# Performance work log

Hardware: AMD Instinct MI355X
Metric: run time of the kernel (lower is better)

## Reference

```python
import jax, jax.numpy as jnp
import numpy as np

B, N0, D0, N1, D1 = 128, 64, 32, 64, 32
K = 65  # depthwise conv kernel size
SCALE = 5.0
FOCUS = 3.0
EPS_Z = float(jnp.finfo(jnp.float32).eps)


def setup_inputs() -> dict:
    key = jax.random.key(0)
    k1, k2, k3, kw, kc, kb = jax.random.split(key, 6)
    x1 = jax.random.normal(k1, (B, N0, D0), dtype=jnp.float32)
    x2 = jax.random.normal(k2, (B, N0, D0), dtype=jnp.float32)
    x3 = jax.random.normal(k3, (B, N0, D0), dtype=jnp.float32)
    # kaiming_normal_ on W [N1, N0, D0, D1]: fan_in = N0*D0*D1 per torch default on 4D
    fan_in = N0 * D0 * D1
    W = jax.random.normal(kw, (N1, N0, D0, D1), dtype=jnp.float32) * np.sqrt(2.0 / fan_in)
    # Conv1d(N1*D1, N1*D1, K, groups=N1): weight [out_ch, in_ch/groups, K]
    cin_g = D1
    bound = 1.0 / np.sqrt(cin_g * K)
    conv_w = jax.random.uniform(kc, (N1 * D1, cin_g, K), dtype=jnp.float32, minval=-bound, maxval=bound)
    conv_b = jax.random.uniform(kb, (N1 * D1,), dtype=jnp.float32, minval=-bound, maxval=bound)
    return {"x1": x1, "x2": x2, "x3": x3, "W": W, "conv_w": conv_w, "conv_b": conv_b}


def _transform(x, W):
    # x: [B, N0, D0], W: [N1, N0, D0, D1] -> u: [B, N1*D1, N0]
    u = jnp.einsum('bji,kjiz->bkjz', x, W)        # [B, N1, N0, D1]
    u = jnp.transpose(u, (0, 1, 3, 2))             # [B, N1, D1, N0]
    return u.reshape(u.shape[0], N1 * D1, N0)


def _focus(u):
    # ReLU kernel + focusing-factor renormalization along last dim
    u = jax.nn.relu(u) + 1e-6
    u = u / SCALE
    n = jnp.linalg.norm(u, axis=-1, keepdims=True)
    up = u ** FOCUS
    return up / jnp.linalg.norm(up, axis=-1, keepdims=True) * n


def _squash(x, eps=1e-20):
    norm = jnp.linalg.norm(x, axis=-1, keepdims=True)
    coef = 1.0 - 1.0 / (jnp.exp(norm) + eps)
    return coef * (x / (norm + eps))


def reference(x1, x2, x3, W, conv_w, conv_b):
    u1 = _focus(_transform(x1, W))  # [B, N1*D1, N0]
    u2 = _focus(_transform(x2, W))
    u3 = _focus(_transform(x3, W))
    z = 1.0 / (jnp.einsum('bic,bc->bi', u1, u1.sum(axis=1)) + EPS_Z)  # [B, N1*D1]
    kv = jnp.einsum('bjc,bjd->bcd', u2, u3)                           # [B, N0, N0]
    x = jnp.einsum('bic,bcd,bi->bid', u1, kv, z)                      # [B, N1*D1, N0]
    # grouped (depthwise-per-capsule) conv1d, 'same' padding
    y = jax.lax.conv_general_dilated(
        x, conv_w, window_strides=(1,), padding=[(K // 2, K // 2)],
        dimension_numbers=('NCH', 'OIH', 'NCH'), feature_group_count=N1)
    y = y + conv_b[None, :, None]
    out = (x + y).sum(axis=-1).reshape(-1, N1, D1)  # [B, N1, D1]
    return _squash(out)
```

## Files before the change

### kernel.cpp

```cpp
#include <hip/hip_runtime.h>
#include <cstddef>

#define NB 128
#define NT 64
#define ND 32
#define NG 64
#define NC 2048
#define KW 65
#define EPSZ 1.1920928955078125e-07f

#define OFF_URAW 0ull
#define SZ_URAW  (3ull * NB * NT * NC)
#define OFF_F    (OFF_URAW + SZ_URAW)
#define SZ_F     (3ull * NB * NC)
#define OFF_S1   (OFF_F + SZ_F)
#define SZ_S1    ((unsigned long long)NB * NT)
#define OFF_KV   (OFF_S1 + SZ_S1)
#define SZ_KV    ((unsigned long long)NB * NT * NT)

__device__ __forceinline__ float foc(float v, float fv) {
  float u = (fmaxf(v, 0.f) + 1e-6f) * 0.2f;
  return u * u * u * fv;
}

__global__ __launch_bounds__(256) void k_transform(
    const float* __restrict__ x1, const float* __restrict__ x2,
    const float* __restrict__ x3, const float* __restrict__ W,
    float* __restrict__ uraw) {
  int bid = blockIdx.x;
  int j   = bid & 63;
  int nt  = (bid >> 6) & 15;
  int inp = bid >> 10;
  const float* x = (inp == 0) ? x1 : ((inp == 1) ? x2 : x3);
  float* uout = uraw + (size_t)inp * ((size_t)NB * NT * NC);

  __shared__ float as[32][132];
  __shared__ float bs[32][132];
  int tid = threadIdx.x;

  {
    int b = tid >> 1, h = tid & 1;
    const float* xp = x + ((size_t)b * NT + j) * ND + h * 16;
#pragma unroll
    for (int q = 0; q < 4; ++q) {
      float4 v = *reinterpret_cast<const float4*>(xp + q * 4);
      int i0 = h * 16 + q * 4;
      as[i0 + 0][b] = v.x; as[i0 + 1][b] = v.y;
      as[i0 + 2][b] = v.z; as[i0 + 3][b] = v.w;
    }
  }
  {
    int kk = tid >> 6, u = tid & 63;
    int i = u >> 1, h = u & 1;
    const float* wp = W + (((size_t)(nt * 4 + kk) * NT + j) * ND + i) * ND + h * 16;
#pragma unroll
    for (int q = 0; q < 4; ++q) {
      float4 v = *reinterpret_cast<const float4*>(wp + q * 4);
      int c0 = kk * 32 + h * 16 + q * 4;
      bs[i][c0 + 0] = v.x; bs[i][c0 + 1] = v.y;
      bs[i][c0 + 2] = v.z; bs[i][c0 + 3] = v.w;
    }
  }
  __syncthreads();

  int tm = tid & 15, tn = tid >> 4;
  int m0 = tm * 8, n0 = tn * 8;
  float acc[8][8];
#pragma unroll
  for (int a = 0; a < 8; ++a)
#pragma unroll
    for (int c = 0; c < 8; ++c) acc[a][c] = 0.f;

#pragma unroll 4
  for (int kk = 0; kk < 32; ++kk) {
    float4 a0 = *reinterpret_cast<const float4*>(&as[kk][m0]);
    float4 a1 = *reinterpret_cast<const float4*>(&as[kk][m0 + 4]);
    float4 b0 = *reinterpret_cast<const float4*>(&bs[kk][n0]);
    float4 b1 = *reinterpret_cast<const float4*>(&bs[kk][n0 + 4]);
    float av[8] = {a0.x, a0.y, a0.z, a0.w, a1.x, a1.y, a1.z, a1.w};
    float bv[8] = {b0.x, b0.y, b0.z, b0.w, b1.x, b1.y, b1.z, b1.w};
#pragma unroll
    for (int mi = 0; mi < 8; ++mi)
#pragma unroll
      for (int ni = 0; ni < 8; ++ni)
        acc[mi][ni] = fmaf(av[mi], bv[ni], acc[mi][ni]);
  }

#pragma unroll
  for (int mi = 0; mi < 8; ++mi) {
    float* cp = uout + ((size_t)(m0 + mi) * NT + j) * NC + nt * 128 + n0;
    float4 v0 = {acc[mi][0], acc[mi][1], acc[mi][2], acc[mi][3]};
    float4 v1 = {acc[mi][4], acc[mi][5], acc[mi][6], acc[mi][7]};
    *reinterpret_cast<float4*>(cp)     = v0;
    *reinterpret_cast<float4*>(cp + 4) = v1;
  }
}

__global__ __launch_bounds__(256) void k_factors(
    const float* __restrict__ uraw, float* __restrict__ f,
    float* __restrict__ s1) {
  int bid = blockIdx.x;
  int q = bid & 3, b = (bid >> 2) & 127, inp = bid >> 9;
  const float* u = uraw + ((size_t)inp * NB + b) * ((size_t)NT * NC);
  int tid = threadIdx.x;
  int ch = q * 512 + tid * 2;

  float s2a = 0.f, s6a = 0.f, s2b = 0.f, s6b = 0.f;
  for (int t = 0; t < NT; ++t) {
    float2 v = *reinterpret_cast<const float2*>(u + (size_t)t * NC + ch);
    float ua = (fmaxf(v.x, 0.f) + 1e-6f) * 0.2f;
    float p2a = ua * ua, p3a = p2a * ua;
    s2a += p2a; s6a += p3a * p3a;
    float ub = (fmaxf(v.y, 0.f) + 1e-6f) * 0.2f;
    float p2b = ub * ub, p3b = p2b * ub;
    s2b += p2b; s6b += p3b * p3b;
  }
  float fa = sqrtf(s2a) / sqrtf(s6a);
  float fb = sqrtf(s2b) / sqrtf(s6b);
  float2 fv = {fa, fb};
  *reinterpret_cast<float2*>(f + ((size_t)inp * NB + b) * NC + ch) = fv;

  if (inp == 0) {
    __shared__ float part[NT][4];
    int wid = tid >> 6, lane = tid & 63;
    for (int t = 0; t < NT; ++t) {
      float2 v = *reinterpret_cast<const float2*>(u + (size_t)t * NC + ch);
      float ua = (fmaxf(v.x, 0.f) + 1e-6f) * 0.2f;
      float ub = (fmaxf(v.y, 0.f) + 1e-6f) * 0.2f;
      float val = ua * ua * ua * fa + ub * ub * ub * fb;
#pragma unroll
      for (int m = 32; m >= 1; m >>= 1) val += __shfl_xor(val, m, 64);
      if (lane == 0) part[t][wid] = val;
    }
    __syncthreads();
    if (tid < NT)
      atomicAdd(&s1[b * NT + tid],
                part[tid][0] + part[tid][1] + part[tid][2] + part[tid][3]);
  }
}

__global__ void k_zero(float* __restrict__ p, int n) {
  int i = blockIdx.x * blockDim.x + threadIdx.x;
  int stride = gridDim.x * blockDim.x;
  for (; i < n; i += stride) p[i] = 0.f;
}

__global__ __launch_bounds__(256) void k_kv(
    const float* __restrict__ uraw, const float* __restrict__ f,
    float* __restrict__ kv) {
  int b = blockIdx.x >> 2, ks = blockIdx.x & 3;
  int wv = threadIdx.x >> 6, lane = threadIdx.x & 63;
  const float* u2 = uraw + ((size_t)NB + b) * ((size_t)NT * NC);
  const float* u3 = uraw + (2ull * NB + b) * ((size_t)NT * NC);
  const float* f2 = f + ((size_t)NB + b) * NC;
  const float* f3 = f + (2ull * NB + b) * NC;

  __shared__ float ldsF[16384];
  float* L2 = ldsF + wv * 4096;
  float* L3 = L2 + 2048;

  int tm = lane >> 3, tn = lane & 7;
  int sr = lane >> 3, c4 = lane & 7;

  float acc[8][8];
#pragma unroll
  for (int i = 0; i < 8; ++i)
#pragma unroll
    for (int j = 0; j < 8; ++j) acc[i][j] = 0.f;

  for (int chunk = 0; chunk < 4; ++chunk) {
    int ch0 = ks * 512 + wv * 128 + chunk * 32;
    float4 f2q = *reinterpret_cast<const float4*>(f2 + ch0 + c4 * 4);
    float4 f3q = *reinterpret_cast<const float4*>(f3 + ch0 + c4 * 4);
#pragma unroll
    for (int it = 0; it < 8; ++it) {
      int t = it * 8 + sr;
      int q4s = c4 ^ sr ^ it;
      float4 v2 = *reinterpret_cast<const float4*>(u2 + (size_t)t * NC + ch0 + c4 * 4);
      float4 v3 = *reinterpret_cast<const float4*>(u3 + (size_t)t * NC + ch0 + c4 * 4);
      float4 w2 = {foc(v2.x, f2q.x), foc(v2.y, f2q.y), foc(v2.z, f2q.z), foc(v2.w, f2q.w)};
      float4 w3 = {foc(v3.x, f3q.x), foc(v3.y, f3q.y), foc(v3.z, f3q.z), foc(v3.w, f3q.w)};
      *reinterpret_cast<float4*>(L2 + t * 32 + q4s * 4) = w2;
      *reinterpret_cast<float4*>(L3 + t * 32 + q4s * 4) = w3;
    }

#pragma unroll
    for (int kp = 0; kp < 16; ++kp) {
      int q4 = kp >> 1, h = (kp & 1) * 2;
      float2 af[8], bf[8];
#pragma unroll
      for (int i = 0; i < 8; ++i)
        af[i] = *reinterpret_cast<const float2*>(
            L2 + (tm * 8 + i) * 32 + ((q4 ^ i ^ tm) * 4 + h));
#pragma unroll
      for (int j = 0; j < 8; ++j)
        bf[j] = *reinterpret_cast<const float2*>(
            L3 + (tn * 8 + j) * 32 + ((q4 ^ j ^ tn) * 4 + h));
#pragma unroll
      for (int i = 0; i < 8; ++i)
#pragma unroll
        for (int j = 0; j < 8; ++j)
          acc[i][j] = fmaf(af[i].y, bf[j].y, fmaf(af[i].x, bf[j].x, acc[i][j]));
    }
  }

  __syncthreads();
  if (wv > 0) {
    float* dp = ldsF + (wv - 1) * 4224 + lane * 66;
#pragma unroll
    for (int i = 0; i < 8; ++i)
#pragma unroll
      for (int j = 0; j < 8; ++j) dp[i * 8 + j] = acc[i][j];
  }
  __syncthreads();
  if (wv == 0) {
    float* kvp = kv + (size_t)b * (NT * NT);
    const float* d0 = ldsF + lane * 66;
    const float* d1 = ldsF + 4224 + lane * 66;
    const float* d2 = ldsF + 8448 + lane * 66;
#pragma unroll
    for (int i = 0; i < 8; ++i)
#pragma unroll
      for (int j = 0; j < 8; ++j) {
        int c = i * 8 + j;
        atomicAdd(&kvp[(tm * 8 + i) * 64 + tn * 8 + j],
                  acc[i][j] + d0[c] + d1[c] + d2[c]);
      }
  }
}

__global__ __launch_bounds__(64) void k_cwt(
    const float* __restrict__ cw, float* __restrict__ cwt) {
  int o = blockIdx.x;
  int tid = threadIdx.x;
  __shared__ float row[32 * KW];
  for (int i = tid; i < 32 * KW; i += 64) row[i] = cw[(size_t)o * (32 * KW) + i];
  __syncthreads();
  int jj = tid, j = jj + 1;
  for (int ci = 0; ci < 32; ++ci) {
    float v = 0.f;
    if (j <= 32) v -= row[ci * KW + j + 32];
    if (j >= 32 && j <= 63) v += row[ci * KW + j - 32];
    if (j == 64) {
      float s = 0.f;
      for (int k = 32; k <= 64; ++k) s += row[ci * KW + k];
      v += s;
    }
    cwt[(size_t)o * 2048 + ci * 64 + jj] = v;
  }
}

__global__ __launch_bounds__(256) void k_pre(
    const float* __restrict__ uraw, const float* __restrict__ f,
    const float* __restrict__ kvg, const float* __restrict__ s1g,
    float* __restrict__ pre) {
  int b = blockIdx.x >> 3, q = blockIdx.x & 7;
  int chbase = q * 256;
  const float* u1 = uraw + (size_t)b * ((size_t)NT * NC);
  const float* f1 = f + (size_t)b * NC;
  int tid = threadIdx.x;

  __shared__ float kvpreL[64][68];
  __shared__ float s1L[64];
  __shared__ float utL[64][132];

#pragma unroll
  for (int qq = 0; qq < 16; ++qq) {
    int i = tid + qq * 256;
    kvpreL[i >> 6][i & 63] = kvg[(size_t)b * (NT * NT) + i];
  }
  if (tid < 64) s1L[tid] = s1g[b * NT + tid];
  __syncthreads();
  if (tid < 64) {
    float run = 0.f;
    for (int t2 = 0; t2 < 64; ++t2) {
      run += kvpreL[tid][t2];
      kvpreL[tid][t2] = run;
    }
  }

  int cg = tid >> 3, tg = tid & 7;
  for (int tile = 0; tile < 2; ++tile) {
    int ch0 = chbase + tile * 128;
    __syncthreads();
    {
      int t = tid >> 2, c4 = tid & 3;
      const float* up = u1 + (size_t)t * NC + ch0 + c4 * 32;
      const float* fp = f1 + ch0 + c4 * 32;
#pragma unroll
      for (int qq = 0; qq < 8; ++qq) {
        float4 v  = *reinterpret_cast<const float4*>(up + qq * 4);
        float4 fv = *reinterpret_cast<const float4*>(fp + qq * 4);
        float vv[4] = {v.x, v.y, v.z, v.w};
        float ff[4] = {fv.x, fv.y, fv.z, fv.w};
#pragma unroll
        for (int r = 0; r < 4; ++r) {
          float uu = (fmaxf(vv[r], 0.f) + 1e-6f) * 0.2f;
          utL[t][c4 * 33 + qq * 4 + r] = uu * uu * uu * ff[r];
        }
      }
    }
    __syncthreads();

    int cl = cg * 4;
    int sk = (cl >> 5) * 33 + (cl & 31);
    float acc[4][8];
#pragma unroll
    for (int r = 0; r < 4; ++r)
#pragma unroll
      for (int c = 0; c < 8; ++c) acc[r][c] = 0.f;
    float accz[4] = {0.f, 0.f, 0.f, 0.f};

#pragma unroll 4
    for (int t1 = 0; t1 < 64; ++t1) {
      float4 a = *reinterpret_cast<const float4*>(&utL[t1][sk]);
      float s = s1L[t1];
      float4 k0 = *reinterpret_cast<const float4*>(&kvpreL[t1][tg * 8]);
      float4 k1 = *reinterpret_cast<const float4*>(&kvpreL[t1][tg * 8 + 4]);
      float aa[4] = {a.x, a.y, a.z, a.w};
      float kk[8] = {k0.x, k0.y, k0.z, k0.w, k1.x, k1.y, k1.z, k1.w};
#pragma unroll
      for (int r = 0; r < 4; ++r) {
        accz[r] = fmaf(aa[r], s, accz[r]);
#pragma unroll
        for (int c = 0; c < 8; ++c)
          acc[r][c] = fmaf(aa[r], kk[c], acc[r][c]);
      }
    }
#pragma unroll
    for (int r = 0; r < 4; ++r) {
      float z = 1.f / (accz[r] + EPSZ);
      float* pp = pre + ((size_t)b * NC + ch0 + cl + r) * 64 + tg * 8;
      float4 o0 = {acc[r][0] * z, acc[r][1] * z, acc[r][2] * z, acc[r][3] * z};
      float4 o1 = {acc[r][4] * z, acc[r][5] * z, acc[r][6] * z, acc[r][7] * z};
      *reinterpret_cast<float4*>(pp)     = o0;
      *reinterpret_cast<float4*>(pp + 4) = o1;
    }
  }
}

__global__ __launch_bounds__(256) void k_gemm(
    const float* __restrict__ pre, const float* __restrict__ cwt,
    const float* __restrict__ cb, float* __restrict__ out) {
  int g = blockIdx.x >> 2, bq = blockIdx.x & 3;
  int b0 = bq * 32;
  int tid = threadIdx.x;
  int oh = tid & 15, bh = tid >> 4;

  __shared__ float preL[32][68];
  __shared__ float cwtL[32][68];

  float a00 = 0.f, a01 = 0.f, a10 = 0.f, a11 = 0.f;
  float xs00 = 0.f, xs01 = 0.f, xs10 = 0.f, xs11 = 0.f;

  for (int kc = 0; kc < 32; ++kc) {
    __syncthreads();
    {
      int r8 = tid >> 3, s8 = tid & 7;
      const float* ps = pre + ((size_t)(b0 + r8) * NC + g * 32) * 64 + kc * 64 + s8 * 8;
      float4 p0 = *reinterpret_cast<const float4*>(ps);
      float4 p1 = *reinterpret_cast<const float4*>(ps + 4);
      *reinterpret_cast<float4*>(&preL[r8][s8 * 8])     = p0;
      *reinterpret_cast<float4*>(&preL[r8][s8 * 8 + 4]) = p1;
      const float* cs = cwt + (size_t)(g * 32 + r8) * 2048 + kc * 64 + s8 * 8;
      float4 c0 = *reinterpret_cast<const float4*>(cs);
      float4 c1 = *reinterpret_cast<const float4*>(cs + 4);
      *reinterpret_cast<float4*>(&cwtL[r8][s8 * 8])     = c0;
      *reinterpret_cast<float4*>(&cwtL[r8][s8 * 8 + 4]) = c1;
    }
    __syncthreads();

    if (kc == oh)      { xs00 = preL[bh][63]; xs10 = preL[bh + 16][63]; }
    if (kc == oh + 16) { xs01 = preL[bh][63]; xs11 = preL[bh + 16][63]; }

#pragma unroll
    for (int kk = 0; kk < 64; kk += 4) {
      float4 p0 = *reinterpret_cast<const float4*>(&preL[bh][kk]);
      float4 p1 = *reinterpret_cast<const float4*>(&preL[bh + 16][kk]);
      float4 c0 = *reinterpret_cast<const float4*>(&cwtL[oh][kk]);
      float4 c1 = *reinterpret_cast<const float4*>(&cwtL[oh + 16][kk]);
      a00 = fmaf(p0.x, c0.x, a00); a00 = fmaf(p0.y, c0.y, a00);
      a00 = fmaf(p0.z, c0.z, a00); a00 = fmaf(p0.w, c0.w, a00);
      a01 = fmaf(p0.x, c1.x, a01); a01 = fmaf(p0.y, c1.y, a01);
      a01 = fmaf(p0.z, c1.z, a01); a01 = fmaf(p0.w, c1.w, a01);
      a10 = fmaf(p1.x, c0.x, a10); a10 = fmaf(p1.y, c0.y, a10);
      a10 = fmaf(p1.z, c0.z, a10); a10 = fmaf(p1.w, c0.w, a10);
      a11 = fmaf(p1.x, c1.x, a11); a11 = fmaf(p1.y, c1.y, a11);
      a11 = fmaf(p1.z, c1.z, a11); a11 = fmaf(p1.w, c1.w, a11);
    }
  }

  float cb0 = cb[g * 32 + oh], cb1 = cb[g * 32 + oh + 16];
  float v00 = a00 + xs00 + 64.f * cb0;
  float v01 = a01 + xs01 + 64.f * cb1;
  float v10 = a10 + xs10 + 64.f * cb0;
  float v11 = a11 + xs11 + 64.f * cb1;

  float sqA = v00 * v00 + v01 * v01;
  float sqB = v10 * v10 + v11 * v11;
#pragma unroll
  for (int m = 8; m >= 1; m >>= 1) {
    sqA += __shfl_xor(sqA, m, 16);
    sqB += __shfl_xor(sqB, m, 16);
  }
  float nA = sqrtf(sqA), nB = sqrtf(sqB);
  float cA = 1.f - 1.f / (expf(nA) + 1e-20f);
  float cB = 1.f - 1.f / (expf(nB) + 1e-20f);
  float iA = cA / (nA + 1e-20f), iB = cB / (nB + 1e-20f);

  size_t baseA = ((size_t)(b0 + bh) * NG + g) * ND;
  size_t baseB = ((size_t)(b0 + bh + 16) * NG + g) * ND;
  out[baseA + oh]      = v00 * iA;
  out[baseA + oh + 16] = v01 * iA;
  out[baseB + oh]      = v10 * iB;
  out[baseB + oh + 16] = v11 * iB;
}

extern "C" void kernel_launch(void* const* d_in, const int* in_sizes, int n_in,
                              void* d_out, int out_size, void* d_ws, size_t ws_size,
                              hipStream_t stream) {
  const float* x1 = (const float*)d_in[0];
  const float* x2 = (const float*)d_in[1];
  const float* x3 = (const float*)d_in[2];
  const float* W  = (const float*)d_in[3];
  const float* cw = (const float*)d_in[4];
  const float* cb = (const float*)d_in[5];
  float* out = (float*)d_out;

  float* ws   = (float*)d_ws;
  float* uraw = ws + OFF_URAW;
  float* f    = ws + OFF_F;
  float* s1   = ws + OFF_S1;
  float* kv   = ws + OFF_KV;
  float* pre  = uraw + (size_t)NB * NT * NC;
  float* cwt  = uraw + 2ull * NB * NT * NC;

  k_transform<<<3072, 256, 0, stream>>>(x1, x2, x3, W, uraw);
  k_zero<<<256, 256, 0, stream>>>(s1, (int)(SZ_S1 + SZ_KV));
  k_factors<<<1536, 256, 0, stream>>>(uraw, f, s1);
  k_kv<<<512, 256, 0, stream>>>(uraw, f, kv);
  k_cwt<<<2048, 64, 0, stream>>>(cw, cwt);
  k_pre<<<1024, 256, 0, stream>>>(uraw, f, kv, s1, pre);
  k_gemm<<<256, 256, 0, stream>>>(pre, cwt, cb, out);
}
```

Baseline: 422.9 us.

## Fuse focus-factor computation for inputs 2 and 3 into the kv kernel

After: 412.0 us. 1.03x faster.

```diff
diff --git a/kernel.cpp b/kernel.cpp
--- a/kernel.cpp
+++ b/kernel.cpp
@@ -100,8 +100,8 @@
     const float* __restrict__ uraw, float* __restrict__ f,
     float* __restrict__ s1) {
   int bid = blockIdx.x;
-  int q = bid & 3, b = (bid >> 2) & 127, inp = bid >> 9;
-  const float* u = uraw + ((size_t)inp * NB + b) * ((size_t)NT * NC);
+  int q = bid & 3, b = bid >> 2;
+  const float* u = uraw + (size_t)b * ((size_t)NT * NC);
   int tid = threadIdx.x;
   int ch = q * 512 + tid * 2;
 
@@ -118,25 +118,23 @@
   float fa = sqrtf(s2a) / sqrtf(s6a);
   float fb = sqrtf(s2b) / sqrtf(s6b);
   float2 fv = {fa, fb};
-  *reinterpret_cast<float2*>(f + ((size_t)inp * NB + b) * NC + ch) = fv;
-
-  if (inp == 0) {
-    __shared__ float part[NT][4];
-    int wid = tid >> 6, lane = tid & 63;
-    for (int t = 0; t < NT; ++t) {
-      float2 v = *reinterpret_cast<const float2*>(u + (size_t)t * NC + ch);
-      float ua = (fmaxf(v.x, 0.f) + 1e-6f) * 0.2f;
-      float ub = (fmaxf(v.y, 0.f) + 1e-6f) * 0.2f;
-      float val = ua * ua * ua * fa + ub * ub * ub * fb;
-#pragma unroll
-      for (int m = 32; m >= 1; m >>= 1) val += __shfl_xor(val, m, 64);
-      if (lane == 0) part[t][wid] = val;
-    }
-    __syncthreads();
-    if (tid < NT)
-      atomicAdd(&s1[b * NT + tid],
-                part[tid][0] + part[tid][1] + part[tid][2] + part[tid][3]);
-  }
+  *reinterpret_cast<float2*>(f + (size_t)b * NC + ch) = fv;
+
+  __shared__ float part[NT][4];
+  int wid = tid >> 6, lane = tid & 63;
+  for (int t = 0; t < NT; ++t) {
+    float2 v = *reinterpret_cast<const float2*>(u + (size_t)t * NC + ch);
+    float ua = (fmaxf(v.x, 0.f) + 1e-6f) * 0.2f;
+    float ub = (fmaxf(v.y, 0.f) + 1e-6f) * 0.2f;
+    float val = ua * ua * ua * fa + ub * ub * ub * fb;
+#pragma unroll
+    for (int m = 32; m >= 1; m >>= 1) val += __shfl_xor(val, m, 64);
+    if (lane == 0) part[t][wid] = val;
+  }
+  __syncthreads();
+  if (tid < NT)
+    atomicAdd(&s1[b * NT + tid],
+              part[tid][0] + part[tid][1] + part[tid][2] + part[tid][3]);
 }
 
 __global__ void k_zero(float* __restrict__ p, int n) {
@@ -146,87 +144,105 @@
 }
 
 __global__ __launch_bounds__(256) void k_kv(
-    const float* __restrict__ uraw, const float* __restrict__ f,
-    float* __restrict__ kv) {
-  int b = blockIdx.x >> 2, ks = blockIdx.x & 3;
-  int wv = threadIdx.x >> 6, lane = threadIdx.x & 63;
+    const float* __restrict__ uraw, float* __restrict__ kv) {
+  int b = blockIdx.x >> 3, ks = blockIdx.x & 7;
+  int tid = threadIdx.x;
+  int wv = tid >> 6, lane = tid & 63;
   const float* u2 = uraw + ((size_t)NB + b) * ((size_t)NT * NC);
   const float* u3 = uraw + (2ull * NB + b) * ((size_t)NT * NC);
-  const float* f2 = f + ((size_t)NB + b) * NC;
-  const float* f3 = f + (2ull * NB + b) * NC;
-
-  __shared__ float ldsF[16384];
-  float* L2 = ldsF + wv * 4096;
-  float* L3 = L2 + 2048;
-
+
+  __shared__ float L[2][64][32];
+  __shared__ float fL[2][32];
+
+  int q4 = tid & 7, tr = tid >> 3;
+  int colf = tid >> 1, hf = tid & 1;
+  int opf = colf >> 5, chf = colf & 31, c4f = chf >> 2, clf = chf & 3;
+  int qr = wv >> 1, qc = wv & 1;
   int tm = lane >> 3, tn = lane & 7;
-  int sr = lane >> 3, c4 = lane & 7;
-
-  float acc[8][8];
-#pragma unroll
-  for (int i = 0; i < 8; ++i)
-#pragma unroll
-    for (int j = 0; j < 8; ++j) acc[i][j] = 0.f;
-
-  for (int chunk = 0; chunk < 4; ++chunk) {
-    int ch0 = ks * 512 + wv * 128 + chunk * 32;
-    float4 f2q = *reinterpret_cast<const float4*>(f2 + ch0 + c4 * 4);
-    float4 f3q = *reinterpret_cast<const float4*>(f3 + ch0 + c4 * 4);
-#pragma unroll
-    for (int it = 0; it < 8; ++it) {
-      int t = it * 8 + sr;
-      int q4s = c4 ^ sr ^ it;
-      float4 v2 = *reinterpret_cast<const float4*>(u2 + (size_t)t * NC + ch0 + c4 * 4);
-      float4 v3 = *reinterpret_cast<const float4*>(u3 + (size_t)t * NC + ch0 + c4 * 4);
-      float4 w2 = {foc(v2.x, f2q.x), foc(v2.y, f2q.y), foc(v2.z, f2q.z), foc(v2.w, f2q.w)};
-      float4 w3 = {foc(v3.x, f3q.x), foc(v3.y, f3q.y), foc(v3.z, f3q.z), foc(v3.w, f3q.w)};
-      *reinterpret_cast<float4*>(L2 + t * 32 + q4s * 4) = w2;
-      *reinterpret_cast<float4*>(L3 + t * 32 + q4s * 4) = w3;
-    }
-
+
+  float acc[4][4];
+#pragma unroll
+  for (int i = 0; i < 4; ++i)
+#pragma unroll
+    for (int j = 0; j < 4; ++j) acc[i][j] = 0.f;
+
+  for (int chunk = 0; chunk < 8; ++chunk) {
+    int ch0 = ks * 256 + chunk * 32;
+    __syncthreads();
+#pragma unroll
+    for (int it = 0; it < 2; ++it) {
+      int t = it * 32 + tr;
+      int q4s = q4 ^ (t & 7) ^ (t >> 3);
+      float4 v2 = *reinterpret_cast<const float4*>(u2 + (size_t)t * NC + ch0 + q4 * 4);
+      float4 v3 = *reinterpret_cast<const float4*>(u3 + (size_t)t * NC + ch0 + q4 * 4);
+      *reinterpret_cast<float4*>(&L[0][t][q4s * 4]) = v2;
+      *reinterpret_cast<float4*>(&L[1][t][q4s * 4]) = v3;
+    }
+    __syncthreads();
+    {
+      float s2 = 0.f, s6 = 0.f;
+#pragma unroll
+      for (int k = 0; k < 32; ++k) {
+        int t = hf * 32 + k;
+        float v = L[opf][t][((c4f ^ (t & 7) ^ (t >> 3)) << 2) + clf];
+        float uu = (fmaxf(v, 0.f) + 1e-6f) * 0.2f;
+        float p2 = uu * uu; s2 += p2;
+        float p3 = p2 * uu; s6 += p3 * p3;
+      }
+      s2 += __shfl_xor(s2, 1, 64);
+      s6 += __shfl_xor(s6, 1, 64);
+      if (hf == 0) fL[opf][chf] = sqrtf(s2) / sqrtf(s6);
+    }
+    __syncthreads();
+    {
+      float4 f2q = *reinterpret_cast<const float4*>(&fL[0][q4 * 4]);
+      float4 f3q = *reinterpret_cast<const float4*>(&fL[1][q4 * 4]);
+#pragma unroll
+      for (int it = 0; it < 2; ++it) {
+        int t = it * 32 + tr;
+        int q4s = q4 ^ (t & 7) ^ (t >> 3);
+        float* p2p = &L[0][t][q4s * 4];
+        float* p3p = &L[1][t][q4s * 4];
+        float4 v2 = *reinterpret_cast<const float4*>(p2p);
+        float4 v3 = *reinterpret_cast<const float4*>(p3p);
+        float4 w2 = {foc(v2.x, f2q.x), foc(v2.y, f2q.y), foc(v2.z, f2q.z), foc(v2.w, f2q.w)};
+        float4 w3 = {foc(v3.x, f3q.x), foc(v3.y, f3q.y), foc(v3.z, f3q.z), foc(v3.w, f3q.w)};
+        *reinterpret_cast<float4*>(p2p) = w2;
+        *reinterpret_cast<float4*>(p3p) = w3;
+      }
+    }
+    __syncthreads();
 #pragma unroll
     for (int kp = 0; kp < 16; ++kp) {
-      int q4 = kp >> 1, h = (kp & 1) * 2;
-      float2 af[8], bf[8];
-#pragma unroll
-      for (int i = 0; i < 8; ++i)
+      int qk = kp >> 1, h2 = (kp & 1) * 2;
+      float2 af[4], bf[4];
+#pragma unroll
+      for (int i = 0; i < 4; ++i) {
+        int t1 = qr * 32 + tm * 4 + i;
         af[i] = *reinterpret_cast<const float2*>(
-            L2 + (tm * 8 + i) * 32 + ((q4 ^ i ^ tm) * 4 + h));
-#pragma unroll
-      for (int j = 0; j < 8; ++j)
+            &L[0][t1][((qk ^ (t1 & 7) ^ (t1 >> 3)) << 2) + h2]);
+      }
+#pragma unroll
+      for (int j = 0; j < 4; ++j) {
+        int t2 = qc * 32 + tn * 4 + j;
         bf[j] = *reinterpret_cast<const float2*>(
-            L3 + (tn * 8 + j) * 32 + ((q4 ^ j ^ tn) * 4 + h));
-#pragma unroll
-      for (int i = 0; i < 8; ++i)
-#pragma unroll
-        for (int j = 0; j < 8; ++j)
+            &L[1][t2][((qk ^ (t2 & 7) ^ (t2 >> 3)) << 2) + h2]);
+      }
+#pragma unroll
+      for (int i = 0; i < 4; ++i)
+#pragma unroll
+        for (int j = 0; j < 4; ++j)
           acc[i][j] = fmaf(af[i].y, bf[j].y, fmaf(af[i].x, bf[j].x, acc[i][j]));
     }
   }
 
-  __syncthreads();
-  if (wv > 0) {
-    float* dp = ldsF + (wv - 1) * 4224 + lane * 66;
-#pragma unroll
-    for (int i = 0; i < 8; ++i)
-#pragma unroll
-      for (int j = 0; j < 8; ++j) dp[i * 8 + j] = acc[i][j];
-  }
-  __syncthreads();
-  if (wv == 0) {
-    float* kvp = kv + (size_t)b * (NT * NT);
-    const float* d0 = ldsF + lane * 66;
-    const float* d1 = ldsF + 4224 + lane * 66;
-    const float* d2 = ldsF + 8448 + lane * 66;
-#pragma unroll
-    for (int i = 0; i < 8; ++i)
-#pragma unroll
-      for (int j = 0; j < 8; ++j) {
-        int c = i * 8 + j;
-        atomicAdd(&kvp[(tm * 8 + i) * 64 + tn * 8 + j],
-                  acc[i][j] + d0[c] + d1[c] + d2[c]);
-      }
-  }
+  float* kvp = kv + (size_t)b * (NT * NT);
+#pragma unroll
+  for (int i = 0; i < 4; ++i)
+#pragma unroll
+    for (int j = 0; j < 4; ++j)
+      atomicAdd(&kvp[(qr * 32 + tm * 4 + i) * 64 + qc * 32 + tn * 4 + j],
+                acc[i][j]);
 }
 
 __global__ __launch_bounds__(64) void k_cwt(
@@ -437,8 +453,8 @@
 
   k_transform<<<3072, 256, 0, stream>>>(x1, x2, x3, W, uraw);
   k_zero<<<256, 256, 0, stream>>>(s1, (int)(SZ_S1 + SZ_KV));
-  k_factors<<<1536, 256, 0, stream>>>(uraw, f, s1);
-  k_kv<<<512, 256, 0, stream>>>(uraw, f, kv);
+  k_factors<<<512, 256, 0, stream>>>(uraw, f, s1);
+  k_kv<<<1024, 256, 0, stream>>>(uraw, kv);
   k_cwt<<<2048, 64, 0, stream>>>(cw, cwt);
   k_pre<<<1024, 256, 0, stream>>>(uraw, f, kv, s1, pre);
   k_gemm<<<256, 256, 0, stream>>>(pre, cwt, cb, out);
```
